# Kernel tuning notes

Hardware: AMD Instinct MI355X
Metric: run time of the kernel (lower is better)

The kernel has to match this reference:

```python
import jax, jax.numpy as jnp
import numpy as np

B, S, D, NH = 2, 2048, 1024, 8
DH = D // NH
EPS = 1e-6
LN_EPS = 1e-5


def setup_inputs() -> dict:
    key = jax.random.key(0)
    ks = jax.random.split(key, 8)
    rnd = lambda k, sh, s=1.0: jax.random.normal(k, sh, dtype=jnp.float32) * s
    return {
        "q": rnd(ks[0], (B, S, D)),
        "k": rnd(ks[1], (B, S, D)),
        "v": rnd(ks[2], (B, S, D)),
        "igate_w": rnd(ks[3], (NH, 3 * D), 0.02),
        "igate_b": jnp.linspace(3.0, 6.0, NH, dtype=jnp.float32),
        "fgate_w": rnd(ks[4], (NH, 3 * D), 0.02),
        "fgate_b": rnd(ks[5], (NH,), 0.3162278),
        "ln_scale": jnp.ones((D,), dtype=jnp.float32),
    }


def _mlstm_cell(q, k, v, igate_w, igate_b, fgate_w, fgate_b, ln_scale):
    # q,k,v: [S, D]
    Slen = q.shape[0]
    ifg = jnp.concatenate([q, k, v], axis=-1)            # [S, 3D]
    ig = (ifg @ igate_w.T + igate_b).T                   # [NH, S] input gate preact
    fg = (ifg @ fgate_w.T + fgate_b).T                   # [NH, S] forget gate preact
    qh = q.reshape(Slen, NH, DH).transpose(1, 0, 2)      # [NH, S, DH]
    kh = k.reshape(Slen, NH, DH).transpose(1, 0, 2)
    vh = v.reshape(Slen, NH, DH).transpose(1, 0, 2)

    log_f = jax.nn.log_sigmoid(fg)                       # [NH, S]
    cs = jnp.cumsum(log_f, axis=1)                       # [NH, S]
    # log_fg_matrix[h,i,j] = cs[h,i] - cs[h,j]  (causal only)
    fg_mat = cs[:, :, None] - cs[:, None, :]             # [NH, S, S]
    mask = jnp.tril(jnp.ones((Slen, Slen), dtype=bool))
    log_fg_mat = jnp.where(mask, fg_mat, -jnp.inf)
    log_D = log_fg_mat + ig[:, None, :]                  # add igate of column j
    max_log_D = jnp.max(log_D, axis=-1, keepdims=True)   # row-wise stabilization
    D_mat = jnp.exp(log_D - max_log_D)

    qk = jnp.einsum("hsd,htd->hst", qh, kh) / np.sqrt(DH)
    C = qk * D_mat
    normalizer = jnp.maximum(jnp.abs(C.sum(axis=-1, keepdims=True)), jnp.exp(-max_log_D))
    h = jnp.einsum("hst,htd->hsd", C / (normalizer + EPS), vh)  # [NH, S, DH]
    h = h.transpose(1, 0, 2).reshape(Slen, D)

    mu = h.mean(axis=-1, keepdims=True)
    var = h.var(axis=-1, keepdims=True)
    return (h - mu) / jnp.sqrt(var + LN_EPS) * ln_scale


def reference(q, k, v, igate_w, igate_b, fgate_w, fgate_b, ln_scale):
    return jax.vmap(
        lambda qq, kk, vv: _mlstm_cell(qq, kk, vv, igate_w, igate_b, fgate_w, fgate_b, ln_scale)
    )(q, k, v)
```

## Files before the change

### kernel.cpp

```cpp
#include <hip/hip_runtime.h>
#include <hip/hip_bf16.h>

#define SLEN 2048
#define DMODEL 1024
#define NHEAD 8
#define DHEAD 128
#define BM 64
#define BKT 64
#define QSCALE 0.08838834764831845f

typedef __attribute__((ext_vector_type(4))) float f32x4;
typedef __attribute__((ext_vector_type(8))) _Float16 f16x8;
typedef __attribute__((ext_vector_type(4))) _Float16 f16x4;
typedef __attribute__((ext_vector_type(2))) _Float16 f16x2;

static __device__ __forceinline__ int pk16(float a, float b) {
  f16x2 t; t[0] = (_Float16)a; t[1] = (_Float16)b;
  union { f16x2 h; int i; } u; u.h = t; return u.i;
}
static __device__ __forceinline__ unsigned short f16bits(float x) {
  union { _Float16 h; unsigned short u; } u2; u2.h = (_Float16)x; return u2.u;
}

__global__ __launch_bounds__(512)
void gates_kernel(const float* __restrict__ q, const float* __restrict__ k,
                  const float* __restrict__ v, const float* __restrict__ igw,
                  const float* __restrict__ fgw, float* __restrict__ gpre) {
  __shared__ float red[8][16][16];
  const int row0 = blockIdx.x * 16;
  const int tid = threadIdx.x;
  const int lane = tid & 63, wid = tid >> 6;
  const int l15 = lane & 15, lg = lane >> 4;
  const f32x4 z4 = {0.f, 0.f, 0.f, 0.f};
  f32x4 acc = z4;
  const float* wbase = (l15 < 8) ? (igw + (size_t)l15 * 3072)
                                 : (fgw + (size_t)(l15 - 8) * 3072);
  #pragma unroll
  for (int ks = 0; ks < 12; ++ks) {
    const int kk = wid * 384 + ks * 32 + lg * 8;
    const int seg = kk >> 10;
    const int col = kk & 1023;
    const float* src = (seg == 0) ? q : (seg == 1) ? k : v;
    const float* xp = src + (size_t)(row0 + l15) * 1024 + col;
    f32x4 a0 = *(const f32x4*)xp;
    f32x4 a1 = *(const f32x4*)(xp + 4);
    f32x4 b0 = *(const f32x4*)(wbase + kk);
    f32x4 b1 = *(const f32x4*)(wbase + kk + 4);
    f16x8 ah, al, bhf, blf;
    #pragma unroll
    for (int e = 0; e < 4; ++e) {
      _Float16 h0 = (_Float16)a0[e], h1 = (_Float16)a1[e];
      ah[e] = h0; ah[e + 4] = h1;
      al[e] = (_Float16)(a0[e] - (float)h0);
      al[e + 4] = (_Float16)(a1[e] - (float)h1);
      _Float16 g0 = (_Float16)b0[e], g1 = (_Float16)b1[e];
      bhf[e] = g0; bhf[e + 4] = g1;
      blf[e] = (_Float16)(b0[e] - (float)g0);
      blf[e + 4] = (_Float16)(b1[e] - (float)g1);
    }
    acc = __builtin_amdgcn_mfma_f32_16x16x32_f16(ah, bhf, acc, 0, 0, 0);
    acc = __builtin_amdgcn_mfma_f32_16x16x32_f16(al, bhf, acc, 0, 0, 0);
    acc = __builtin_amdgcn_mfma_f32_16x16x32_f16(ah, blf, acc, 0, 0, 0);
  }
  #pragma unroll
  for (int r = 0; r < 4; ++r)
    red[wid][lg * 4 + r][l15] = acc[r];
  __syncthreads();
  if (tid < 256) {
    const int xrow = tid >> 4, g = tid & 15;
    float s = 0.f;
    #pragma unroll
    for (int w = 0; w < 8; ++w) s += red[w][xrow][g];
    gpre[(size_t)g * 4096 + row0 + xrow] = s;
  }
}

__global__ __launch_bounds__(256)
void scan_kernel(const float* __restrict__ gpre, const float* __restrict__ igb,
                 const float* __restrict__ fgb, float* __restrict__ a_out,
                 float* __restrict__ ms_out, float* __restrict__ fl_out,
                 float* __restrict__ mt64, float* __restrict__ mt128,
                 float* __restrict__ Mg_out) {
  const int bh = blockIdx.x;
  const int h = bh & 7;
  const int b = bh >> 3;
  const int tid = threadIdx.x;
  __shared__ double sbd[256];
  __shared__ float sbf[256];
  __shared__ float mt_l[16];
  const int base = b * 2048 + tid * 8;
  const float ig_b = igb[h], fg_b = fgb[h];
  double cs[8];
  float av[8];
  double tot = 0.0;
  #pragma unroll
  for (int e = 0; e < 8; ++e) {
    float x = gpre[(size_t)(8 + h) * 4096 + base + e] + fg_b;
    float l = fminf(x, 0.f) - log1pf(__expf(-fabsf(x)));
    tot += (double)l;
    cs[e] = tot;
  }
  sbd[tid] = tot;
  __syncthreads();
  if (tid == 0) {
    double run = 0.0;
    for (int i = 0; i < 256; ++i) { double t2 = sbd[i]; sbd[i] = run; run += t2; }
  }
  __syncthreads();
  const double excl = sbd[tid];
  float mtot = -3.4e38f;
  #pragma unroll
  for (int e = 0; e < 8; ++e) {
    cs[e] += excl;
    float ig = gpre[(size_t)h * 4096 + base + e] + ig_b;
    av[e] = (float)((double)ig - cs[e]);
    mtot = fmaxf(mtot, av[e]);
  }
  {
    float w8 = mtot;
    w8 = fmaxf(w8, __shfl_xor(w8, 1));
    w8 = fmaxf(w8, __shfl_xor(w8, 2));
    w8 = fmaxf(w8, __shfl_xor(w8, 4));
    if ((tid & 7) == 0) mt64[bh * 32 + (tid >> 3)] = w8;
    float w16 = fmaxf(w8, __shfl_xor(w8, 8));
    if ((tid & 15) == 0) { mt128[bh * 16 + (tid >> 4)] = w16; mt_l[tid >> 4] = w16; }
  }
  sbf[tid] = mtot;
  __syncthreads();
  if (tid == 0) {
    float run = -3.4e38f;
    for (int i = 0; i < 256; ++i) { float t2 = sbf[i]; sbf[i] = run; run = fmaxf(run, t2); }
    float M = -3.4e38f;
    for (int c = 0; c < 16; ++c) { Mg_out[bh * 16 + c] = M; M = fmaxf(M, mt_l[c]); }
  }
  __syncthreads();
  float run = sbf[tid];
  const int obase = bh * 2048 + tid * 8;
  #pragma unroll
  for (int e = 0; e < 8; ++e) {
    run = fmaxf(run, av[e]);
    a_out[obase + e] = av[e];
    ms_out[obase + e] = run;
    fl_out[obase + e] = __expf(-(float)(cs[e] + (double)run));
  }
}

__global__ __launch_bounds__(512)
void p1_kernel(const float* __restrict__ k, const float* __restrict__ v,
               const float* __restrict__ a_g, const float* __restrict__ mt128,
               unsigned short* __restrict__ GXs, float* __restrict__ pkt) {
  __shared__ __align__(16) char pool[33280];
  _Float16* Kts = (_Float16*)pool;
  _Float16* Vts = (_Float16*)(pool + 16384);
  float* w_s = (float*)(pool + 32768);
  const int c = blockIdx.x, bh = blockIdx.y;
  const int b = bh >> 3, h = bh & 7;
  const int tid = threadIdx.x;
  const int lane = tid & 63, wid = tid >> 6;
  const int l15 = lane & 15, lg = lane >> 4;
  if (tid < 128) w_s[tid] = __expf(a_g[bh * SLEN + c * 128 + tid] - mt128[bh * 16 + c]);
  const f32x4 z4 = {0.f, 0.f, 0.f, 0.f};
  f32x4 acc[8];
  #pragma unroll
  for (int i = 0; i < 8; ++i) acc[i] = z4;
  float ks_acc = 0.f;
  for (int p = 0; p < 2; ++p) {
    const int j0 = c * 128 + p * 64;
    __syncthreads();
    {
      const int d = tid & 127;
      const int jq = tid >> 7;
      const size_t rowb = (size_t)(b * SLEN + j0 + jq * 16) * DMODEL + h * DHEAD + d;
      float kv[16], vv[16];
      #pragma unroll
      for (int jj = 0; jj < 16; ++jj) {
        kv[jj] = k[rowb + (size_t)jj * DMODEL] * w_s[p * 64 + jq * 16 + jj];
        vv[jj] = v[rowb + (size_t)jj * DMODEL];
      }
      int ph[8], pv[8];
      #pragma unroll
      for (int pp = 0; pp < 8; ++pp) {
        ph[pp] = pk16(kv[2 * pp], kv[2 * pp + 1]);
        pv[pp] = pk16(vv[2 * pp], vv[2 * pp + 1]);
      }
      const int sw = (d & 7) << 4;
      const int b0 = d * 128 + jq * 32;
      *(f32x4*)((char*)Kts + ((b0 + 0) ^ sw))  = *(f32x4*)&ph[0];
      *(f32x4*)((char*)Kts + ((b0 + 16) ^ sw)) = *(f32x4*)&ph[4];
      *(f32x4*)((char*)Vts + ((b0 + 0) ^ sw))  = *(f32x4*)&pv[0];
      *(f32x4*)((char*)Vts + ((b0 + 16) ^ sw)) = *(f32x4*)&pv[4];
    }
    __syncthreads();
    f16x8 avv[2];
    {
      const int row = wid * 16 + l15;
      const int sw = (l15 & 7) << 4;
      avv[0] = *(const f16x8*)((char*)Vts + row * 128 + ((lg * 16) ^ sw));
      avv[1] = *(const f16x8*)((char*)Vts + row * 128 + ((64 + lg * 16) ^ sw));
    }
    #pragma unroll
    for (int dkt = 0; dkt < 8; ++dkt) {
      const int row = dkt * 16 + l15;
      const int sw = (l15 & 7) << 4;
      #pragma unroll
      for (int ks = 0; ks < 2; ++ks) {
        const int bc = ks * 64 + lg * 16;
        f16x8 bh8 = *(const f16x8*)((char*)Kts + row * 128 + (bc ^ sw));
        acc[dkt] = __builtin_amdgcn_mfma_f32_16x16x32_f16(avv[ks], bh8, acc[dkt], 0, 0, 0);
      }
    }
    if (tid < 128) {
      const int sw = (tid & 7) << 4;
      #pragma unroll
      for (int g = 0; g < 8; ++g) {
        f16x8 hh = *(const f16x8*)((char*)Kts + tid * 128 + ((g * 16) ^ sw));
        #pragma unroll
        for (int e = 0; e < 8; ++e) ks_acc += (float)hh[e];
      }
    }
  }
  unsigned short* gxs = GXs + (size_t)(bh * 16 + c) * 16384;
  #pragma unroll
  for (int dkt = 0; dkt < 8; ++dkt)
    #pragma unroll
    for (int r = 0; r < 4; ++r)
      gxs[(wid * 16 + lg * 4 + r) * 128 + dkt * 16 + l15] = f16bits(acc[dkt][r]);
  if (tid < 128) pkt[(size_t)(bh * 16 + c) * 128 + tid] = ks_acc;
}

__global__ __launch_bounds__(256)
void p2_kernel(const float* __restrict__ mt128, unsigned short* __restrict__ GXs,
               const float* __restrict__ pkt, float* __restrict__ pkx) {
  const int s = blockIdx.x, bh = blockIdx.y;
  const int tid = threadIdx.x;
  union U8 { uint4 q; _Float16 h[8]; };
  if (s < 8) {
    unsigned short* base = GXs + (size_t)bh * 16 * 16384 + s * 2048 + tid * 8;
    float X[8];
    #pragma unroll
    for (int e = 0; e < 8; ++e) X[e] = 0.f;
    float Mm1 = -3.4e38f;
    for (int c = 0; c < 16; ++c) {
      U8 cu; cu.q = *(const uint4*)(base + (size_t)c * 16384);
      const float mtc = mt128[bh * 16 + c];
      const float Mc = fmaxf(Mm1, mtc);
      const float s1 = __expf(Mm1 - Mc), s2 = __expf(mtc - Mc);
      U8 ou;
      #pragma unroll
      for (int e = 0; e < 8; ++e) ou.h[e] = (_Float16)X[e];
      *(uint4*)(base + (size_t)c * 16384) = ou.q;
      #pragma unroll
      for (int e = 0; e < 8; ++e) X[e] = X[e] * s1 + (float)cu.h[e] * s2;
      Mm1 = Mc;
    }
  } else if (tid < 128) {
    const float* pb = pkt + (size_t)bh * 16 * 128 + tid;
    float X = 0.f, Mm1 = -3.4e38f;
    for (int c = 0; c < 16; ++c) {
      const float g = pb[(size_t)c * 128];
      const float mtc = mt128[bh * 16 + c];
      const float Mc = fmaxf(Mm1, mtc);
      pkx[(size_t)bh * 16 * 128 + (size_t)c * 128 + tid] = X;
      X = X * __expf(Mm1 - Mc) + g * __expf(mtc - Mc);
      Mm1 = Mc;
    }
  }
}

__global__ __launch_bounds__(1024)
__attribute__((amdgpu_waves_per_eu(4, 4)))
void p3_kernel(const float* __restrict__ q, const float* __restrict__ k,
               const float* __restrict__ v, const float* __restrict__ a_g,
               const float* __restrict__ ms_g, const float* __restrict__ fl_g,
               const float* __restrict__ Mg_g, const float* __restrict__ pkx,
               const unsigned short* __restrict__ GXs, float* __restrict__ out) {
  __shared__ __align__(16) char pool[50944];
  _Float16* Ks_hi = (_Float16*)pool;
  _Float16* Ks_lo = (_Float16*)(pool + 16384);
  _Float16* Vts   = (_Float16*)(pool + 32768);
  float* a_s      = (float*)(pool + 49152);
  float* rs_lds   = (float*)(pool + 49408);
  float* pks      = (float*)(pool + 50432);
  float* hex      = (float*)pool;

  const int bid = blockIdx.x;
  const int c = bid & 15;
  const int bh = bid >> 4;
  const int b = bh >> 3, h = bh & 7;
  const int tid = threadIdx.x;
  const int lane = tid & 63;
  const int wid = tid >> 6;
  const int tt = wid >> 3;
  const int wr = (wid >> 1) & 3;
  const int wc = wid & 1;
  const int l15 = lane & 15;
  const int lg = lane >> 4;
  const int t = 2 * c + tt;
  const int i0 = t * BM;
  const f32x4 z4 = {0.f, 0.f, 0.f, 0.f};

  f16x8 qh[4], ql[4];
  {
    const float* qbase = q + (size_t)(b * SLEN + i0 + wr * 16 + l15) * DMODEL + h * DHEAD;
    #pragma unroll
    for (int ks = 0; ks < 4; ++ks) {
      f32x4 x0 = *(const f32x4*)(qbase + ks * 32 + lg * 8);
      f32x4 x1 = *(const f32x4*)(qbase + ks * 32 + lg * 8 + 4);
      f16x8 hi, lo;
      #pragma unroll
      for (int e = 0; e < 4; ++e) {
        float s0 = x0[e] * QSCALE, s1 = x1[e] * QSCALE;
        _Float16 h0 = (_Float16)s0, h1 = (_Float16)s1;
        hi[e] = h0;     hi[e + 4] = h1;
        lo[e] = (_Float16)(s0 - (float)h0);
        lo[e + 4] = (_Float16)(s1 - (float)h1);
      }
      qh[ks] = hi; ql[ks] = lo;
    }
  }
  const float m_reg = ms_g[bh * SLEN + i0 + wr * 16 + l15];
  const float fl_reg = fl_g[bh * SLEN + i0 + wr * 16 + l15];
  const float e_l = __expf(Mg_g[bh * 16 + c] - m_reg);

  f32x4 hacc[8];
  #pragma unroll
  for (int cf = 0; cf < 8; ++cf) hacc[cf] = z4;
  float ps = 0.f;

  if (c > 0) {
    const char* gxs = (const char*)(GXs + (size_t)(bh * 16 + c) * 16384);
    const int xrow = tid >> 3;
    const int xcb = (tid & 7) * 32;
    const int sw = (xrow & 7) << 4;
    uint4 g0 = *(const uint4*)(gxs + xrow * 256 + xcb);
    uint4 g1 = *(const uint4*)(gxs + xrow * 256 + xcb + 16);
    *(uint4*)((char*)pool + xrow * 256 + ((xcb + 0) ^ sw)) = g0;
    *(uint4*)((char*)pool + xrow * 256 + ((xcb + 16) ^ sw)) = g1;
  }
  if (tid < 128) pks[tid] = pkx[(size_t)(bh * 16 + c) * 128 + tid];
  __syncthreads();

  if (c > 0) {
    f16x8 qe[2];
    #pragma unroll
    for (int kss = 0; kss < 2; ++kss) {
      const int ks = wc * 2 + kss;
      #pragma unroll
      for (int e = 0; e < 8; ++e)
        qe[kss][e] = (_Float16)(((float)qh[ks][e] + (float)ql[ks][e]) * e_l);
    }
    #pragma unroll
    for (int cf = 0; cf < 8; ++cf) {
      const int row = cf * 16 + l15;
      const int sw = (row & 7) << 4;
      #pragma unroll
      for (int kss = 0; kss < 2; ++kss) {
        const int bc = (wc * 2 + kss) * 64 + lg * 16;
        f16x8 xh = *(const f16x8*)((char*)pool + row * 256 + (bc ^ sw));
        hacc[cf] = __builtin_amdgcn_mfma_f32_16x16x32_f16(qe[kss], xh, hacc[cf], 0, 0, 0);
      }
    }
    if (wc == 0) {
      float dot = 0.f;
      #pragma unroll
      for (int ks = 0; ks < 4; ++ks)
        #pragma unroll
        for (int e = 0; e < 8; ++e)
          dot += ((float)qh[ks][e] + (float)ql[ks][e]) * pks[ks * 32 + lg * 8 + e];
      ps += dot * e_l;
    }
  }

  #pragma unroll
  for (int pss = 0; pss < 2; ++pss) {
    const int j0 = c * 128 + pss * 64;
    __syncthreads();

    {
      const int krow = tid >> 4;
      const int kc0 = (tid & 15) * 8;
      const float* kp = k + (size_t)(b * SLEN + j0 + krow) * DMODEL + h * DHEAD + kc0;
      char* bh_ = (char*)Ks_hi + krow * 256;
      char* bl_ = (char*)Ks_lo + krow * 256;
      const int sw = (krow & 7) << 4;
      #pragma unroll
      for (int e = 0; e < 2; ++e) {
        f32x4 xv = *(const f32x4*)(kp + e * 4);
        f16x4 hi, lo;
        #pragma unroll
        for (int u = 0; u < 4; ++u) {
          _Float16 hh = (_Float16)xv[u];
          hi[u] = hh; lo[u] = (_Float16)(xv[u] - (float)hh);
        }
        const int bc = (kc0 + e * 4) * 2;
        *(f16x4*)(bh_ + (bc ^ sw)) = hi;
        *(f16x4*)(bl_ + (bc ^ sw)) = lo;
      }
    }
    {
      const int d = tid & 127;
      const int jq = tid >> 7;
      const float* vp = v + (size_t)(b * SLEN + j0 + jq * 8) * DMODEL + h * DHEAD + d;
      float vv[8];
      #pragma unroll
      for (int jj = 0; jj < 8; ++jj)
        vv[jj] = vp[(size_t)jj * DMODEL];
      int pv[4];
      #pragma unroll
      for (int p = 0; p < 4; ++p) pv[p] = pk16(vv[2 * p], vv[2 * p + 1]);
      const int sw = (d & 7) << 4;
      const int b0 = d * 128 + jq * 16;
      *(f32x4*)((char*)Vts + (b0 ^ sw)) = *(f32x4*)&pv[0];
    }
    if (tid < BKT) a_s[tid] = a_g[bh * SLEN + j0 + tid];
    __syncthreads();

    if (pss <= tt) {
      f32x4 sacc[2];
      sacc[0] = z4; sacc[1] = z4;
      #pragma unroll
      for (int ks = 0; ks < 4; ++ks) {
        const int bc = ks * 64 + lg * 16;
        #pragma unroll
        for (int jfl = 0; jfl < 2; ++jfl) {
          const int arow = wc * 32 + jfl * 16 + l15;
          const int sw = (arow & 7) << 4;
          f16x8 kh8 = *(const f16x8*)((char*)Ks_hi + arow * 256 + (bc ^ sw));
          f16x8 kl8 = *(const f16x8*)((char*)Ks_lo + arow * 256 + (bc ^ sw));
          sacc[jfl] = __builtin_amdgcn_mfma_f32_16x16x32_f16(kh8, qh[ks], sacc[jfl], 0, 0, 0);
          sacc[jfl] = __builtin_amdgcn_mfma_f32_16x16x32_f16(kl8, qh[ks], sacc[jfl], 0, 0, 0);
          sacc[jfl] = __builtin_amdgcn_mfma_f32_16x16x32_f16(kh8, ql[ks], sacc[jfl], 0, 0, 0);
        }
      }
      float vals[2][4];
      {
        const int iG = i0 + wr * 16 + l15;
        #pragma unroll
        for (int jfl = 0; jfl < 2; ++jfl)
          #pragma unroll
          for (int r = 0; r < 4; ++r) {
            const int jl = wc * 32 + jfl * 16 + lg * 4 + r;
            float e = __expf(fminf(a_s[jl] - m_reg, 0.f));
            float vv = sacc[jfl][r] * e;
            if (j0 + jl > iG) vv = 0.f;
            ps += vv;
            vals[jfl][r] = vv;
          }
      }
      const int lgand1 = lg & 1;
      const int idxA = (l15 + 16 * (2 * lgand1 + 0)) * 4;
      const int idxB = (l15 + 16 * (2 * lgand1 + 1)) * 4;
      const bool hi_half = ((lane & 63) >= 32);
      int c2[2][2];
      #pragma unroll
      for (int jfl = 0; jfl < 2; ++jfl) {
        c2[jfl][0] = pk16(vals[jfl][0], vals[jfl][1]);
        c2[jfl][1] = pk16(vals[jfl][2], vals[jfl][3]);
      }
      int pa32[4];
      #pragma unroll
      for (int p = 0; p < 4; ++p) {
        const int idx2 = (p < 2) ? idxA : idxB;
        int f0 = __builtin_amdgcn_ds_bpermute(idx2, c2[0][p & 1]);
        int f1 = __builtin_amdgcn_ds_bpermute(idx2, c2[1][p & 1]);
        pa32[p] = hi_half ? f1 : f0;
      }
      union { int i[4]; f16x8 v; } pu;
      pu.i[0] = pa32[0]; pu.i[1] = pa32[1]; pu.i[2] = pa32[2]; pu.i[3] = pa32[3];
      const f16x8 paf = pu.v;

      const int vbc = wc * 64 + lg * 16;
      #pragma unroll
      for (int cf = 0; cf < 8; ++cf) {
        const int vrow = cf * 16 + l15;
        const int sw = (vrow & 7) << 4;
        f16x8 vb8 = *(const f16x8*)((char*)Vts + vrow * 128 + (vbc ^ sw));
        hacc[cf] = __builtin_amdgcn_mfma_f32_16x16x32_f16(paf, vb8, hacc[cf], 0, 0, 0);
      }
    }
  }
  __syncthreads();

  ps += __shfl_xor(ps, 16);
  ps += __shfl_xor(ps, 32);
  if (lane < 16) rs_lds[(tt * 64 + wr * 16 + l15) * 2 + wc] = ps;
  if (tt == 0 && wc == 1) {
    #pragma unroll
    for (int cf = 0; cf < 8; ++cf)
      *(f32x4*)&hex[wr * 2048 + cf * 256 + lane * 4] = hacc[cf];
  }
  __syncthreads();
  if (tt == 0 && wc == 0) {
    #pragma unroll
    for (int cf = 0; cf < 8; ++cf) {
      f32x4 o = *(const f32x4*)&hex[wr * 2048 + cf * 256 + lane * 4];
      hacc[cf][0] += o[0]; hacc[cf][1] += o[1];
      hacc[cf][2] += o[2]; hacc[cf][3] += o[3];
    }
    const float rsum = rs_lds[(wr * 16 + l15) * 2 + 0] + rs_lds[(wr * 16 + l15) * 2 + 1];
    const float inv = 1.0f / (fmaxf(fabsf(rsum), fl_reg) + 1e-6f);
    union { float f; int i; } uc; uc.f = inv;
    float invr[4];
    #pragma unroll
    for (int r = 0; r < 4; ++r) {
      union { float f; int i; } ur;
      ur.i = __builtin_amdgcn_ds_bpermute((lg * 4 + r) * 4, uc.i);
      invr[r] = ur.f;
    }
    #pragma unroll
    for (int r = 0; r < 4; ++r) {
      const size_t orow = (size_t)(b * SLEN + i0 + wr * 16 + lg * 4 + r) * DMODEL + h * DHEAD;
      #pragma unroll
      for (int cf = 0; cf < 8; ++cf)
        out[orow + cf * 16 + l15] = hacc[cf][r] * invr[r];
    }
  }
  __syncthreads();
  if (tt == 1 && wc == 1) {
    #pragma unroll
    for (int cf = 0; cf < 8; ++cf)
      *(f32x4*)&hex[wr * 2048 + cf * 256 + lane * 4] = hacc[cf];
  }
  __syncthreads();
  if (tt == 1 && wc == 0) {
    #pragma unroll
    for (int cf = 0; cf < 8; ++cf) {
      f32x4 o = *(const f32x4*)&hex[wr * 2048 + cf * 256 + lane * 4];
      hacc[cf][0] += o[0]; hacc[cf][1] += o[1];
      hacc[cf][2] += o[2]; hacc[cf][3] += o[3];
    }
    const float rsum = rs_lds[(64 + wr * 16 + l15) * 2 + 0] + rs_lds[(64 + wr * 16 + l15) * 2 + 1];
    const float inv = 1.0f / (fmaxf(fabsf(rsum), fl_reg) + 1e-6f);
    union { float f; int i; } uc; uc.f = inv;
    float invr[4];
    #pragma unroll
    for (int r = 0; r < 4; ++r) {
      union { float f; int i; } ur;
      ur.i = __builtin_amdgcn_ds_bpermute((lg * 4 + r) * 4, uc.i);
      invr[r] = ur.f;
    }
    #pragma unroll
    for (int r = 0; r < 4; ++r) {
      const size_t orow = (size_t)(b * SLEN + i0 + wr * 16 + lg * 4 + r) * DMODEL + h * DHEAD;
      #pragma unroll
      for (int cf = 0; cf < 8; ++cf)
        out[orow + cf * 16 + l15] = hacc[cf][r] * invr[r];
    }
  }
}

__global__ __launch_bounds__(512)
void mlstm_main(const float* __restrict__ q, const float* __restrict__ k,
                const float* __restrict__ v, const float* __restrict__ a_g,
                const float* __restrict__ ms_g, const float* __restrict__ fl_g,
                const float* __restrict__ mt_g, float* __restrict__ out) {
  __shared__ __align__(16) char pool[50176];
  _Float16* Ks_hi = (_Float16*)pool;
  _Float16* Ks_lo = (_Float16*)(pool + 16384);
  _Float16* Vts   = (_Float16*)(pool + 32768);
  float* a_s      = (float*)(pool + 49152);
  float* rs_lds   = (float*)(pool + 49408);
  float* hex      = (float*)pool;

  const int bid = blockIdx.x;
  int t, bh;
  if (bid < 256) { t = 31 - (bid >> 4); bh = bid & 15; }
  else           { t = (bid - 256) >> 4; bh = (bid - 256) & 15; }
  const int b = bh >> 3, h = bh & 7;
  const int i0 = t * BM;
  const int tid = threadIdx.x;
  const int lane = tid & 63;
  const int wid = tid >> 6;
  const int wr = wid >> 1;
  const int wc = wid & 1;
  const int l15 = lane & 15;
  const int lg = lane >> 4;
  const f32x4 z4 = {0.f, 0.f, 0.f, 0.f};

  f16x8 qh[4], ql[4];
  {
    const float* qbase = q + (size_t)(b * SLEN + i0 + wr * 16 + l15) * DMODEL + h * DHEAD;
    #pragma unroll
    for (int ks = 0; ks < 4; ++ks) {
      f32x4 x0 = *(const f32x4*)(qbase + ks * 32 + lg * 8);
      f32x4 x1 = *(const f32x4*)(qbase + ks * 32 + lg * 8 + 4);
      f16x8 hi, lo;
      #pragma unroll
      for (int e = 0; e < 4; ++e) {
        float s0 = x0[e] * QSCALE, s1 = x1[e] * QSCALE;
        _Float16 h0 = (_Float16)s0, h1 = (_Float16)s1;
        hi[e] = h0;     hi[e + 4] = h1;
        lo[e] = (_Float16)(s0 - (float)h0);
        lo[e + 4] = (_Float16)(s1 - (float)h1);
      }
      qh[ks] = hi; ql[ks] = lo;
    }
  }
  const float m_reg = ms_g[bh * SLEN + i0 + wr * 16 + l15];
  const float fl_reg = fl_g[bh * SLEN + i0 + wr * 16 + l15];
  const int lgand1 = lg & 1;
  const int idxA = (l15 + 16 * (2 * lgand1 + 0)) * 4;
  const int idxB = (l15 + 16 * (2 * lgand1 + 1)) * 4;
  const bool hi_half = (lane >= 32);

  f32x4 hacc[8];
  #pragma unroll
  for (int cf = 0; cf < 8; ++cf) hacc[cf] = z4;
  float ps = 0.f;

  const int krow = tid >> 3;
  const int kc0 = (tid & 7) * 16;
  const int vdv = tid & 127;
  const int vjq = tid >> 7;

  for (int jt = 0; jt <= t; ++jt) {
    const int j0 = jt * BKT;
    const bool diag = (jt == t);
    const float mt = mt_g[bh * 32 + jt];
    {
      float es = 1.f;
      if (!diag) es = __expf(a_g[bh * SLEN + j0 + krow] - mt);
      const float* kp = k + (size_t)(b * SLEN + j0 + krow) * DMODEL + h * DHEAD + kc0;
      char* bh_ = (char*)Ks_hi + krow * 256;
      char* bl_ = (char*)Ks_lo + krow * 256;
      const int sw = (krow & 7) << 4;
      #pragma unroll
      for (int e = 0; e < 4; ++e) {
        f32x4 xv = *(const f32x4*)(kp + e * 4);
        f16x4 hi, lo;
        #pragma unroll
        for (int u = 0; u < 4; ++u) {
          float vv = xv[u] * es;
          _Float16 hh = (_Float16)vv;
          hi[u] = hh; lo[u] = (_Float16)(vv - (float)hh);
        }
        const int bc = (kc0 + e * 4) * 2;
        *(f16x4*)(bh_ + (bc ^ sw)) = hi;
        *(f16x4*)(bl_ + (bc ^ sw)) = lo;
      }
    }
    {
      const float* vp = v + (size_t)(b * SLEN + j0 + vjq * 16) * DMODEL + h * DHEAD + vdv;
      float vv[16];
      #pragma unroll
      for (int jj = 0; jj < 16; ++jj)
        vv[jj] = vp[(size_t)jj * DMODEL];
      int pk[8];
      #pragma unroll
      for (int p = 0; p < 8; ++p) pk[p] = pk16(vv[2 * p], vv[2 * p + 1]);
      const int sw = (vdv & 7) << 4;
      *(f32x4*)((char*)Vts + ((vdv * 128 + vjq * 32 + 0) ^ sw)) = *(f32x4*)&pk[0];
      *(f32x4*)((char*)Vts + ((vdv * 128 + vjq * 32 + 16) ^ sw)) = *(f32x4*)&pk[4];
    }
    if (diag && tid < BKT) a_s[tid] = a_g[bh * SLEN + j0 + tid];
    __syncthreads();

    f32x4 sacc[2];
    sacc[0] = z4; sacc[1] = z4;
    #pragma unroll
    for (int ks = 0; ks < 4; ++ks) {
      const int bc = ks * 64 + lg * 16;
      #pragma unroll
      for (int jfl = 0; jfl < 2; ++jfl) {
        const int arow = wc * 32 + jfl * 16 + l15;
        const int sw = (arow & 7) << 4;
        f16x8 kh8 = *(const f16x8*)((char*)Ks_hi + arow * 256 + (bc ^ sw));
        f16x8 kl8 = *(const f16x8*)((char*)Ks_lo + arow * 256 + (bc ^ sw));
        sacc[jfl] = __builtin_amdgcn_mfma_f32_16x16x32_f16(kh8, qh[ks], sacc[jfl], 0, 0, 0);
        sacc[jfl] = __builtin_amdgcn_mfma_f32_16x16x32_f16(kl8, qh[ks], sacc[jfl], 0, 0, 0);
        sacc[jfl] = __builtin_amdgcn_mfma_f32_16x16x32_f16(kh8, ql[ks], sacc[jfl], 0, 0, 0);
      }
    }
    float vals[2][4];
    if (diag) {
      const int iG = i0 + wr * 16 + l15;
      #pragma unroll
      for (int jfl = 0; jfl < 2; ++jfl)
        #pragma unroll
        for (int r = 0; r < 4; ++r) {
          const int jl = wc * 32 + jfl * 16 + lg * 4 + r;
          float e = __expf(fminf(a_s[jl] - m_reg, 0.f));
          float vv = sacc[jfl][r] * e;
          if (j0 + jl > iG) vv = 0.f;
          vals[jfl][r] = vv;
        }
    } else {
      const float em = __expf(fminf(mt - m_reg, 0.f));
      #pragma unroll
      for (int jfl = 0; jfl < 2; ++jfl)
        #pragma unroll
        for (int r = 0; r < 4; ++r)
          vals[jfl][r] = sacc[jfl][r] * em;
    }
    #pragma unroll
    for (int jfl = 0; jfl < 2; ++jfl)
      #pragma unroll
      for (int r = 0; r < 4; ++r) ps += vals[jfl][r];

    int c2[2][2];
    #pragma unroll
    for (int jfl = 0; jfl < 2; ++jfl) {
      c2[jfl][0] = pk16(vals[jfl][0], vals[jfl][1]);
      c2[jfl][1] = pk16(vals[jfl][2], vals[jfl][3]);
    }
    int pa32[4];
    #pragma unroll
    for (int p = 0; p < 4; ++p) {
      const int idx = (p < 2) ? idxA : idxB;
      int f0 = __builtin_amdgcn_ds_bpermute(idx, c2[0][p & 1]);
      int f1 = __builtin_amdgcn_ds_bpermute(idx, c2[1][p & 1]);
      pa32[p] = hi_half ? f1 : f0;
    }
    union { int i[4]; f16x8 v; } pu;
    pu.i[0] = pa32[0]; pu.i[1] = pa32[1]; pu.i[2] = pa32[2]; pu.i[3] = pa32[3];
    const f16x8 paf = pu.v;

    const int vbc = wc * 64 + lg * 16;
    #pragma unroll
    for (int cf = 0; cf < 8; ++cf) {
      const int vrow = cf * 16 + l15;
      const int sw = (vrow & 7) << 4;
      f16x8 vb8 = *(const f16x8*)((char*)Vts + vrow * 128 + (vbc ^ sw));
      hacc[cf] = __builtin_amdgcn_mfma_f32_16x16x32_f16(paf, vb8, hacc[cf], 0, 0, 0);
    }
    __syncthreads();
  }

  ps += __shfl_xor(ps, 16);
  ps += __shfl_xor(ps, 32);
  if (lane < 16) rs_lds[(wr * 16 + l15) * 2 + wc] = ps;
  if (wc == 1) {
    #pragma unroll
    for (int cf = 0; cf < 8; ++cf)
      *(f32x4*)&hex[wr * 2048 + cf * 256 + lane * 4] = hacc[cf];
  }
  __syncthreads();
  if (wc == 0) {
    #pragma unroll
    for (int cf = 0; cf < 8; ++cf) {
      f32x4 o = *(const f32x4*)&hex[wr * 2048 + cf * 256 + lane * 4];
      hacc[cf][0] += o[0]; hacc[cf][1] += o[1];
      hacc[cf][2] += o[2]; hacc[cf][3] += o[3];
    }
    const float rsum = rs_lds[(wr * 16 + l15) * 2 + 0] + rs_lds[(wr * 16 + l15) * 2 + 1];
    const float inv = 1.0f / (fmaxf(fabsf(rsum), fl_reg) + 1e-6f);
    union { float f; int i; } uc; uc.f = inv;
    float invr[4];
    #pragma unroll
    for (int r = 0; r < 4; ++r) {
      union { float f; int i; } ur;
      ur.i = __builtin_amdgcn_ds_bpermute((lg * 4 + r) * 4, uc.i);
      invr[r] = ur.f;
    }
    #pragma unroll
    for (int r = 0; r < 4; ++r) {
      const size_t orow = (size_t)(b * SLEN + i0 + wr * 16 + lg * 4 + r) * DMODEL + h * DHEAD;
      #pragma unroll
      for (int cf = 0; cf < 8; ++cf)
        out[orow + cf * 16 + l15] = hacc[cf][r] * invr[r];
    }
  }
}

__global__ __launch_bounds__(256)
void ln_kernel(float* __restrict__ out, const float* __restrict__ gamma) {
  const int row = blockIdx.x;
  const int tid = threadIdx.x;
  float* x = out + (size_t)row * DMODEL;
  f32x4 xv = ((const f32x4*)x)[tid];
  float s = xv[0] + xv[1] + xv[2] + xv[3];
  float qq = xv[0] * xv[0] + xv[1] * xv[1] + xv[2] * xv[2] + xv[3] * xv[3];
  #pragma unroll
  for (int m = 1; m < 64; m <<= 1) { s += __shfl_xor(s, m); qq += __shfl_xor(qq, m); }
  __shared__ float ss[4], sq[4];
  const int wid = tid >> 6;
  if ((tid & 63) == 0) { ss[wid] = s; sq[wid] = qq; }
  __syncthreads();
  s = ss[0] + ss[1] + ss[2] + ss[3];
  qq = sq[0] + sq[1] + sq[2] + sq[3];
  const float mu = s * (1.f / 1024.f);
  const float var = qq * (1.f / 1024.f) - mu * mu;
  const float rstd = rsqrtf(var + 1e-5f);
  f32x4 g = ((const f32x4*)gamma)[tid];
  f32x4 ov;
  ov[0] = (xv[0] - mu) * rstd * g[0];
  ov[1] = (xv[1] - mu) * rstd * g[1];
  ov[2] = (xv[2] - mu) * rstd * g[2];
  ov[3] = (xv[3] - mu) * rstd * g[3];
  ((f32x4*)x)[tid] = ov;
}

extern "C" void kernel_launch(void* const* d_in, const int* in_sizes, int n_in,
                              void* d_out, int out_size, void* d_ws, size_t ws_size,
                              hipStream_t stream) {
  (void)in_sizes; (void)n_in; (void)out_size;
  const float* q   = (const float*)d_in[0];
  const float* k   = (const float*)d_in[1];
  const float* v   = (const float*)d_in[2];
  const float* igw = (const float*)d_in[3];
  const float* igb = (const float*)d_in[4];
  const float* fgw = (const float*)d_in[5];
  const float* fgb = (const float*)d_in[6];
  const float* lns = (const float*)d_in[7];
  float* out = (float*)d_out;

  float* gpre  = (float*)d_ws;
  float* a_g   = gpre + 65536;
  float* ms_g  = a_g + 32768;
  float* fl_g  = ms_g + 32768;
  float* mt64  = fl_g + 32768;
  float* mt128 = mt64 + 512;
  float* Mg_g  = mt128 + 256;
  float* pkt   = Mg_g + 256;
  float* pkx   = pkt + 32768;
  unsigned short* GXs = (unsigned short*)(pkx + 32768);

  const bool big = ws_size >= (size_t)10 * 1024 * 1024;

  gates_kernel<<<dim3(256), dim3(512), 0, stream>>>(q, k, v, igw, fgw, gpre);
  scan_kernel<<<dim3(16), dim3(256), 0, stream>>>(gpre, igb, fgb, a_g, ms_g, fl_g,
                                                  mt64, mt128, Mg_g);
  if (big) {
    p1_kernel<<<dim3(16, 16), dim3(512), 0, stream>>>(k, v, a_g, mt128, GXs, pkt);
    p2_kernel<<<dim3(9, 16), dim3(256), 0, stream>>>(mt128, GXs, pkt, pkx);
    p3_kernel<<<dim3(256), dim3(1024), 0, stream>>>(q, k, v, a_g, ms_g, fl_g,
                                                    Mg_g, pkx, GXs, out);
  } else {
    mlstm_main<<<dim3(512), dim3(512), 0, stream>>>(q, k, v, a_g, ms_g, fl_g, mt64, out);
  }
  ln_kernel<<<dim3(4096), dim3(256), 0, stream>>>(out, lns);
}
```

Baseline: 82.92 us.

## Stage both K/V tiles and GX state in LDS up front to cut barriers

p3_kernel now loads both 64-row K/V chunks, the inter-chunk state tile, the gate values and pk vectors into separate LDS regions at once, behind a single barrier. The inter-chunk and intra-chunk MFMA phases then run back to back without the per-pass __syncthreads pairs. This removes barrier stalls and lets global loads for all tiles be in flight together. LDS use grows from about 50KB to 130KB per block, which is fine for one 1024-thread block per CU but raises register pressure from holding more loads in flight.

```diff
diff --git a/kernel.cpp b/kernel.cpp
--- a/kernel.cpp
+++ b/kernel.cpp
@@ -274,14 +274,13 @@
                const float* __restrict__ ms_g, const float* __restrict__ fl_g,
                const float* __restrict__ Mg_g, const float* __restrict__ pkx,
                const unsigned short* __restrict__ GXs, float* __restrict__ out) {
-  __shared__ __align__(16) char pool[50944];
-  _Float16* Ks_hi = (_Float16*)pool;
-  _Float16* Ks_lo = (_Float16*)(pool + 16384);
-  _Float16* Vts   = (_Float16*)(pool + 32768);
-  float* a_s      = (float*)(pool + 49152);
-  float* rs_lds   = (float*)(pool + 49408);
-  float* pks      = (float*)(pool + 50432);
-  float* hex      = (float*)pool;
+  __shared__ __align__(16) char pool[133120];
+  float* a_s0   = (float*)(pool + 131072);
+  float* a_s1   = (float*)(pool + 131328);
+  float* rs_lds = (float*)(pool + 131584);
+  float* pks    = (float*)(pool + 132608);
+  float* hex    = (float*)pool;
+  char* const Xb = pool + 98304;
 
   const int bid = blockIdx.x;
   const int c = bid & 15;
@@ -327,61 +326,16 @@
   for (int cf = 0; cf < 8; ++cf) hacc[cf] = z4;
   float ps = 0.f;
 
-  if (c > 0) {
-    const char* gxs = (const char*)(GXs + (size_t)(bh * 16 + c) * 16384);
-    const int xrow = tid >> 3;
-    const int xcb = (tid & 7) * 32;
-    const int sw = (xrow & 7) << 4;
-    uint4 g0 = *(const uint4*)(gxs + xrow * 256 + xcb);
-    uint4 g1 = *(const uint4*)(gxs + xrow * 256 + xcb + 16);
-    *(uint4*)((char*)pool + xrow * 256 + ((xcb + 0) ^ sw)) = g0;
-    *(uint4*)((char*)pool + xrow * 256 + ((xcb + 16) ^ sw)) = g1;
-  }
-  if (tid < 128) pks[tid] = pkx[(size_t)(bh * 16 + c) * 128 + tid];
-  __syncthreads();
-
-  if (c > 0) {
-    f16x8 qe[2];
-    #pragma unroll
-    for (int kss = 0; kss < 2; ++kss) {
-      const int ks = wc * 2 + kss;
-      #pragma unroll
-      for (int e = 0; e < 8; ++e)
-        qe[kss][e] = (_Float16)(((float)qh[ks][e] + (float)ql[ks][e]) * e_l);
-    }
-    #pragma unroll
-    for (int cf = 0; cf < 8; ++cf) {
-      const int row = cf * 16 + l15;
-      const int sw = (row & 7) << 4;
-      #pragma unroll
-      for (int kss = 0; kss < 2; ++kss) {
-        const int bc = (wc * 2 + kss) * 64 + lg * 16;
-        f16x8 xh = *(const f16x8*)((char*)pool + row * 256 + (bc ^ sw));
-        hacc[cf] = __builtin_amdgcn_mfma_f32_16x16x32_f16(qe[kss], xh, hacc[cf], 0, 0, 0);
-      }
-    }
-    if (wc == 0) {
-      float dot = 0.f;
-      #pragma unroll
-      for (int ks = 0; ks < 4; ++ks)
-        #pragma unroll
-        for (int e = 0; e < 8; ++e)
-          dot += ((float)qh[ks][e] + (float)ql[ks][e]) * pks[ks * 32 + lg * 8 + e];
-      ps += dot * e_l;
-    }
-  }
-
   #pragma unroll
   for (int pss = 0; pss < 2; ++pss) {
     const int j0 = c * 128 + pss * 64;
-    __syncthreads();
-
+    char* KB = pool + pss * 49152;
     {
       const int krow = tid >> 4;
       const int kc0 = (tid & 15) * 8;
       const float* kp = k + (size_t)(b * SLEN + j0 + krow) * DMODEL + h * DHEAD + kc0;
-      char* bh_ = (char*)Ks_hi + krow * 256;
-      char* bl_ = (char*)Ks_lo + krow * 256;
+      char* bh_ = KB + krow * 256;
+      char* bl_ = KB + 16384 + krow * 256;
       const int sw = (krow & 7) << 4;
       #pragma unroll
       for (int e = 0; e < 2; ++e) {
@@ -410,12 +364,61 @@
       for (int p = 0; p < 4; ++p) pv[p] = pk16(vv[2 * p], vv[2 * p + 1]);
       const int sw = (d & 7) << 4;
       const int b0 = d * 128 + jq * 16;
-      *(f32x4*)((char*)Vts + (b0 ^ sw)) = *(f32x4*)&pv[0];
-    }
-    if (tid < BKT) a_s[tid] = a_g[bh * SLEN + j0 + tid];
-    __syncthreads();
-
+      *(f32x4*)(KB + 32768 + (b0 ^ sw)) = *(f32x4*)&pv[0];
+    }
+  }
+  if (tid < 64) a_s0[tid] = a_g[bh * SLEN + c * 128 + tid];
+  else if (tid < 128) a_s1[tid - 64] = a_g[bh * SLEN + c * 128 + tid];
+  else if (tid < 256) pks[tid - 128] = pkx[(size_t)(bh * 16 + c) * 128 + (tid - 128)];
+  if (c > 0) {
+    const char* gxs = (const char*)(GXs + (size_t)(bh * 16 + c) * 16384);
+    const int xrow = tid >> 3;
+    const int xcb = (tid & 7) * 32;
+    const int sw = (xrow & 7) << 4;
+    uint4 g0 = *(const uint4*)(gxs + xrow * 256 + xcb);
+    uint4 g1 = *(const uint4*)(gxs + xrow * 256 + xcb + 16);
+    *(uint4*)(Xb + xrow * 256 + ((xcb + 0) ^ sw)) = g0;
+    *(uint4*)(Xb + xrow * 256 + ((xcb + 16) ^ sw)) = g1;
+  }
+  __syncthreads();
+
+  if (c > 0) {
+    f16x8 qe[2];
+    #pragma unroll
+    for (int kss = 0; kss < 2; ++kss) {
+      const int ks = wc * 2 + kss;
+      #pragma unroll
+      for (int e = 0; e < 8; ++e)
+        qe[kss][e] = (_Float16)(((float)qh[ks][e] + (float)ql[ks][e]) * e_l);
+    }
+    #pragma unroll
+    for (int cf = 0; cf < 8; ++cf) {
+      const int row = cf * 16 + l15;
+      const int sw = (row & 7) << 4;
+      #pragma unroll
+      for (int kss = 0; kss < 2; ++kss) {
+        const int bc = (wc * 2 + kss) * 64 + lg * 16;
+        f16x8 xh = *(const f16x8*)(Xb + row * 256 + (bc ^ sw));
+        hacc[cf] = __builtin_amdgcn_mfma_f32_16x16x32_f16(qe[kss], xh, hacc[cf], 0, 0, 0);
+      }
+    }
+    if (wc == 0) {
+      float dot = 0.f;
+      #pragma unroll
+      for (int ks = 0; ks < 4; ++ks)
+        #pragma unroll
+        for (int e = 0; e < 8; ++e)
+          dot += ((float)qh[ks][e] + (float)ql[ks][e]) * pks[ks * 32 + lg * 8 + e];
+      ps += dot * e_l;
+    }
+  }
+
+  #pragma unroll
+  for (int pss = 0; pss < 2; ++pss) {
     if (pss <= tt) {
+      const int j0 = c * 128 + pss * 64;
+      const char* KB = pool + pss * 49152;
+      const float* a_s = (pss == 0) ? a_s0 : a_s1;
       f32x4 sacc[2];
       sacc[0] = z4; sacc[1] = z4;
       #pragma unroll
@@ -425,8 +428,8 @@
         for (int jfl = 0; jfl < 2; ++jfl) {
           const int arow = wc * 32 + jfl * 16 + l15;
           const int sw = (arow & 7) << 4;
-          f16x8 kh8 = *(const f16x8*)((char*)Ks_hi + arow * 256 + (bc ^ sw));
-          f16x8 kl8 = *(const f16x8*)((char*)Ks_lo + arow * 256 + (bc ^ sw));
+          f16x8 kh8 = *(const f16x8*)(KB + arow * 256 + (bc ^ sw));
+          f16x8 kl8 = *(const f16x8*)(KB + 16384 + arow * 256 + (bc ^ sw));
           sacc[jfl] = __builtin_amdgcn_mfma_f32_16x16x32_f16(kh8, qh[ks], sacc[jfl], 0, 0, 0);
           sacc[jfl] = __builtin_amdgcn_mfma_f32_16x16x32_f16(kl8, qh[ks], sacc[jfl], 0, 0, 0);
           sacc[jfl] = __builtin_amdgcn_mfma_f32_16x16x32_f16(kh8, ql[ks], sacc[jfl], 0, 0, 0);
@@ -474,7 +477,7 @@
       for (int cf = 0; cf < 8; ++cf) {
         const int vrow = cf * 16 + l15;
         const int sw = (vrow & 7) << 4;
-        f16x8 vb8 = *(const f16x8*)((char*)Vts + vrow * 128 + (vbc ^ sw));
+        f16x8 vb8 = *(const f16x8*)(KB + 32768 + vrow * 128 + (vbc ^ sw));
         hacc[cf] = __builtin_amdgcn_mfma_f32_16x16x32_f16(paf, vb8, hacc[cf], 0, 0, 0);
       }
     }
```

After: 81.06 us. -2.2%, faster.
